# Performance work log

Hardware: AMD Instinct MI355X
Metric: run time of the kernel (lower is better)

Reference implementation:

```python
import jax, jax.numpy as jnp
import numpy as np

OUT_H = 7
OUT_W = 7
SPATIAL_SCALE = 0.0625
SAMPLING_RATIO = 2  # grid points per bin edge (static, as in Detectron2 configs)
ALIGNED = True


def setup_inputs() -> dict:
    key = jax.random.key(0)
    k_feat, k_xy, k_b = jax.random.split(key, 3)
    N, C, H, W = 2, 256, 128, 128
    K = 1024
    feat = jax.random.normal(k_feat, (N, C, H, W), dtype=jnp.float32)
    img = H / SPATIAL_SCALE  # 2048.0, image-space extent
    # two random corners per axis, sorted -> valid boxes in image coords
    xy = jax.random.uniform(k_xy, (K, 2, 2), dtype=jnp.float32) * img  # [K, {x,y}, 2]
    lo = jnp.min(xy, axis=-1)
    hi = jnp.max(xy, axis=-1)
    b = jax.random.randint(k_b, (K,), 0, N).astype(jnp.float32)
    rois = jnp.stack([b, lo[:, 0], lo[:, 1], hi[:, 0], hi[:, 1]], axis=1)  # [K,5]
    return {"feat": feat, "rois": rois}


def _roi_align(feat, rois):
    N, C, H, W = feat.shape
    K = rois.shape[0]
    g = SAMPLING_RATIO
    b = rois[:, 0].astype(jnp.int32)
    off = 0.5 if ALIGNED else 0.0
    x1 = rois[:, 1] * SPATIAL_SCALE - off
    y1 = rois[:, 2] * SPATIAL_SCALE - off
    x2 = rois[:, 3] * SPATIAL_SCALE - off
    y2 = rois[:, 4] * SPATIAL_SCALE - off
    rw = x2 - x1
    rh = y2 - y1
    if not ALIGNED:  # legacy: force min size 1
        rw = jnp.maximum(rw, 1.0)
        rh = jnp.maximum(rh, 1.0)
    bin_w = rw / OUT_W
    bin_h = rh / OUT_H
    # sample offsets within a bin: (i + 0.5)/g for i in 0..g-1
    frac = (jnp.arange(g, dtype=feat.dtype) + 0.5) / g  # [g]
    ph = jnp.arange(OUT_H, dtype=feat.dtype)
    pw = jnp.arange(OUT_W, dtype=feat.dtype)
    ys = y1[:, None, None] + (ph[None, :, None] + frac[None, None, :]) * bin_h[:, None, None]  # [K,PH,g]
    xs = x1[:, None, None] + (pw[None, :, None] + frac[None, None, :]) * bin_w[:, None, None]  # [K,PW,g]
    ys = ys.reshape(K, OUT_H * g)  # [K,Sy]
    xs = xs.reshape(K, OUT_W * g)  # [K,Sx]
    Y = jnp.broadcast_to(ys[:, :, None], (K, OUT_H * g, OUT_W * g))
    X = jnp.broadcast_to(xs[:, None, :], (K, OUT_H * g, OUT_W * g))
    S = OUT_H * g * OUT_W * g
    Y = Y.reshape(K, S)
    X = X.reshape(K, S)
    valid = (Y > -1.0) & (Y < H) & (X > -1.0) & (X < W)
    Yc = jnp.maximum(Y, 0.0)
    Xc = jnp.maximum(X, 0.0)
    y0 = jnp.clip(jnp.floor(Yc).astype(jnp.int32), 0, H - 1)
    x0 = jnp.clip(jnp.floor(Xc).astype(jnp.int32), 0, W - 1)
    y1i = jnp.minimum(y0 + 1, H - 1)
    x1i = jnp.minimum(x0 + 1, W - 1)
    ly = jnp.clip(Yc - y0.astype(feat.dtype), 0.0, 1.0)
    lx = jnp.clip(Xc - x0.astype(feat.dtype), 0.0, 1.0)
    hy = 1.0 - ly
    hx = 1.0 - lx
    bI = b[:, None]  # [K,1] broadcasts against [K,S]
    # advanced indices around the channel slice put (K,S) in front -> [K,S,C]
    v00 = feat[bI, :, y0, x0]
    v01 = feat[bI, :, y0, x1i]
    v10 = feat[bI, :, y1i, x0]
    v11 = feat[bI, :, y1i, x1i]
    w00 = (hy * hx)[:, :, None]
    w01 = (hy * lx)[:, :, None]
    w10 = (ly * hx)[:, :, None]
    w11 = (ly * lx)[:, :, None]
    val = w00 * v00 + w01 * v01 + w10 * v10 + w11 * v11  # [K,S,C]
    val = jnp.where(valid[:, :, None], val, 0.0)
    val = val.reshape(K, OUT_H, g, OUT_W, g, C)
    out = val.mean(axis=(2, 4))  # avg pool over the g*g samples per bin
    return out.transpose(0, 3, 1, 2)  # [K,C,OUT_H,OUT_W]


def reference(feat, rois):
    return _roi_align(feat, rois)
```

## Files before the change

### kernel.cpp

```cpp
#include <hip/hip_runtime.h>
#include <hip/hip_fp16.h>

#define NIMG 2
#define CCH 256
#define FH 128
#define FW 128
#define FHW (FH * FW)
#define OUTH 7
#define OUTW 7
#define NPIX 49
#define NSAMP (NPIX * 4)
#define KROIS 1024
#define SCALE 0.0625f
#define OPITCH 260

typedef float f32x4 __attribute__((ext_vector_type(4)));

__global__ __launch_bounds__(256) void prep_fused(const float* __restrict__ in,
                                                  __half* __restrict__ out,
                                                  const float* __restrict__ rois,
                                                  int* __restrict__ perm) {
    const int bid = blockIdx.x;
    const int t = threadIdx.x;
    if (bid < 8192) {
        __shared__ float tile[32][33];
        const int b   = bid >> 12;
        const int rem = bid & 4095;
        const int c0  = (rem >> 9) << 5;
        const int hw0 = (rem & 511) << 5;
        const int tx = t & 31;
        const int ty = t >> 5;
        const float* src = in  + (size_t)b * CCH * FHW;
        __half*      dst = out + (size_t)b * FHW * CCH;
#pragma unroll
        for (int i = 0; i < 32; i += 8)
            tile[ty + i][tx] = src[(size_t)(c0 + ty + i) * FHW + hw0 + tx];
        __syncthreads();
#pragma unroll
        for (int i = 0; i < 32; i += 8)
            dst[(size_t)(hw0 + ty + i) * CCH + c0 + tx] = __float2half(tile[tx][ty + i]);
    } else {
        __shared__ int hist[128];
        __shared__ int basep[128];
        __shared__ int keyv[KROIS];
        __shared__ int rankv[KROIS];
        if (t < 128) hist[t] = 0;
        __syncthreads();
#pragma unroll
        for (int i = 0; i < 4; ++i) {
            const int roi = t + (i << 8);
            const float* r = rois + roi * 5;
            const int b = (int)r[0];
            const float cx = (r[1] + r[3]) * 0.5f * SCALE;
            const float cy = (r[2] + r[4]) * 0.5f * SCALE;
            const int qx = min(max((int)cx, 0), FW - 1) >> 4;
            const int qy = min(max((int)cy, 0), FH - 1) >> 4;
            unsigned m = 0;
#pragma unroll
            for (int j = 0; j < 3; ++j)
                m |= (((unsigned)(qx >> j) & 1u) << (2 * j)) | (((unsigned)(qy >> j) & 1u) << (2 * j + 1));
            const int key = (b << 6) | (int)m;
            keyv[roi] = key;
            rankv[roi] = atomicAdd(&hist[key], 1);
        }
        __syncthreads();
        if (t < 64) {
            const int a = hist[2 * t], c = hist[2 * t + 1];
            int s = a + c;
#pragma unroll
            for (int d = 1; d < 64; d <<= 1) {
                const int n = __shfl_up(s, d);
                if (t >= d) s += n;
            }
            const int excl = s - (a + c);
            basep[2 * t]     = excl;
            basep[2 * t + 1] = excl + a;
        }
        __syncthreads();
#pragma unroll
        for (int i = 0; i < 4; ++i) {
            const int roi = t + (i << 8);
            perm[basep[keyv[roi]] + rankv[roi]] = roi;
        }
    }
}

__global__ __launch_bounds__(512) void roi_align_nhwc(const __half* __restrict__ nhwc,
                                                      const float* __restrict__ rois,
                                                      const int* __restrict__ perm,
                                                      float* __restrict__ out) {
    __shared__ __half obuf[NPIX * OPITCH];
    __shared__ __align__(16) int   soff[NSAMP][4];
    __shared__ __align__(16) float swgt[NSAMP][4];
    const int wg = blockIdx.x;
    const int pairBase = ((((wg & 7) << 6) | (wg >> 3)) << 1);
    const int lane = threadIdx.x & 63;
    const int wave = threadIdx.x >> 6;
    const int t = threadIdx.x;

    for (int half = 0; half < 2; ++half) {
        const int k = perm[pairBase + half];
        const float* r = rois + k * 5;
        const int b = __builtin_amdgcn_readfirstlane((int)r[0]);

        if (t < NSAMP) {
            const float x1 = __fsub_rn(__fmul_rn(r[1], SCALE), 0.5f);
            const float y1 = __fsub_rn(__fmul_rn(r[2], SCALE), 0.5f);
            const float x2 = __fsub_rn(__fmul_rn(r[3], SCALE), 0.5f);
            const float y2 = __fsub_rn(__fmul_rn(r[4], SCALE), 0.5f);
            const float bw = __fdiv_rn(__fsub_rn(x2, x1), (float)OUTW);
            const float bh = __fdiv_rn(__fsub_rn(y2, y1), (float)OUTH);
            const int pix = t >> 2, s = t & 3;
            const int ph = pix / 7, pw = pix - ph * 7;
            const int sy = s >> 1, sx = s & 1;
            const float fy = (float)ph + (sy ? 0.75f : 0.25f);
            const float fx = (float)pw + (sx ? 0.75f : 0.25f);
            const float y = __fadd_rn(y1, __fmul_rn(fy, bh));
            const float x = __fadd_rn(x1, __fmul_rn(fx, bw));
            int o00 = 0, o01 = 0, o10 = 0, o11 = 0;
            float w00 = 0.f, w01 = 0.f, w10 = 0.f, w11 = 0.f;
            if (y > -1.0f && y < (float)FH && x > -1.0f && x < (float)FW) {
                const float yc = fmaxf(y, 0.0f);
                const float xc = fmaxf(x, 0.0f);
                int y0 = (int)yc; if (y0 > FH - 1) y0 = FH - 1;
                int x0 = (int)xc; if (x0 > FW - 1) x0 = FW - 1;
                const int y1i = min(y0 + 1, FH - 1);
                const int x1i = min(x0 + 1, FW - 1);
                const float ly = fminf(yc - (float)y0, 1.0f);
                const float lx = fminf(xc - (float)x0, 1.0f);
                const float hy = 1.0f - ly, hx = 1.0f - lx;
                w00 = hy * hx; w01 = hy * lx; w10 = ly * hx; w11 = ly * lx;
                o00 = (y0  * FW + x0 ) << 9;
                o01 = (y0  * FW + x1i) << 9;
                o10 = (y1i * FW + x0 ) << 9;
                o11 = (y1i * FW + x1i) << 9;
            }
            soff[t][0] = o00; soff[t][1] = o01; soff[t][2] = o10; soff[t][3] = o11;
            swgt[t][0] = w00; swgt[t][1] = w01; swgt[t][2] = w10; swgt[t][3] = w11;
        }
        __syncthreads();

        const char* bp = (const char*)(nhwc + ((size_t)b * FHW << 8)) + (lane << 3);
        const int pstart = wave ? (6 * wave + 1) : 0;
        const int pend   = 6 * wave + 6;
        for (int pix = pstart; pix <= pend; ++pix) {
            float acc0 = 0.f, acc1 = 0.f, acc2 = 0.f, acc3 = 0.f;
#pragma unroll
            for (int s = 0; s < 4; ++s) {
                const int j = (pix << 2) + s;
                const int4  o = *(const int4*)(&soff[j][0]);
                const f32x4 w = *(const f32x4*)(&swgt[j][0]);
                const uint2 r00 = *(const uint2*)(bp + o.x);
                const uint2 r01 = *(const uint2*)(bp + o.y);
                const uint2 r10 = *(const uint2*)(bp + o.z);
                const uint2 r11 = *(const uint2*)(bp + o.w);
                const __half2 A00 = *(const __half2*)&r00.x, B00 = *(const __half2*)&r00.y;
                const __half2 A01 = *(const __half2*)&r01.x, B01 = *(const __half2*)&r01.y;
                const __half2 A10 = *(const __half2*)&r10.x, B10 = *(const __half2*)&r10.y;
                const __half2 A11 = *(const __half2*)&r11.x, B11 = *(const __half2*)&r11.y;
                acc0 = fmaf(w.x, __half2float(A00.x), acc0);
                acc1 = fmaf(w.x, __half2float(A00.y), acc1);
                acc2 = fmaf(w.x, __half2float(B00.x), acc2);
                acc3 = fmaf(w.x, __half2float(B00.y), acc3);
                acc0 = fmaf(w.y, __half2float(A01.x), acc0);
                acc1 = fmaf(w.y, __half2float(A01.y), acc1);
                acc2 = fmaf(w.y, __half2float(B01.x), acc2);
                acc3 = fmaf(w.y, __half2float(B01.y), acc3);
                acc0 = fmaf(w.z, __half2float(A10.x), acc0);
                acc1 = fmaf(w.z, __half2float(A10.y), acc1);
                acc2 = fmaf(w.z, __half2float(B10.x), acc2);
                acc3 = fmaf(w.z, __half2float(B10.y), acc3);
                acc0 = fmaf(w.w, __half2float(A11.x), acc0);
                acc1 = fmaf(w.w, __half2float(A11.y), acc1);
                acc2 = fmaf(w.w, __half2float(B11.x), acc2);
                acc3 = fmaf(w.w, __half2float(B11.y), acc3);
            }
            const __half2 h01 = __floats2half2_rn(acc0 * 0.25f, acc1 * 0.25f);
            const __half2 h23 = __floats2half2_rn(acc2 * 0.25f, acc3 * 0.25f);
            uint2 packed;
            packed.x = *(const unsigned*)&h01;
            packed.y = *(const unsigned*)&h23;
            *(uint2*)&obuf[pix * OPITCH + (lane << 2)] = packed;
        }
        __syncthreads();

        float* op = out + (size_t)k * (CCH * NPIX);
        for (int f4 = t; f4 < (CCH * NPIX) / 4; f4 += 512) {
            const int f = f4 << 2;
            f32x4 o;
            {
                const int fi = f + 0; const int c = fi / NPIX; const int p = fi - c * NPIX;
                o.x = __half2float(obuf[p * OPITCH + c]);
            }
            {
                const int fi = f + 1; const int c = fi / NPIX; const int p = fi - c * NPIX;
                o.y = __half2float(obuf[p * OPITCH + c]);
            }
            {
                const int fi = f + 2; const int c = fi / NPIX; const int p = fi - c * NPIX;
                o.z = __half2float(obuf[p * OPITCH + c]);
            }
            {
                const int fi = f + 3; const int c = fi / NPIX; const int p = fi - c * NPIX;
                o.w = __half2float(obuf[p * OPITCH + c]);
            }
            __builtin_nontemporal_store(o, (f32x4*)(op + f));
        }
        __syncthreads();
    }
}

__global__ __launch_bounds__(256) void roi_align_naive(const float* __restrict__ feat,
                                                       const float* __restrict__ rois,
                                                       float* __restrict__ out) {
    const size_t idx = (size_t)blockIdx.x * 256 + threadIdx.x;
    const size_t total = (size_t)KROIS * CCH * NPIX;
    if (idx >= total) return;
    const int pix = (int)(idx % NPIX);
    const int t1  = (int)(idx / NPIX);
    const int c   = t1 % CCH;
    const int k   = t1 / CCH;
    const int ph = pix / 7;
    const int pw = pix - ph * 7;

    const float* r = rois + k * 5;
    const int b = (int)r[0];
    const float x1 = __fsub_rn(__fmul_rn(r[1], SCALE), 0.5f);
    const float y1 = __fsub_rn(__fmul_rn(r[2], SCALE), 0.5f);
    const float x2 = __fsub_rn(__fmul_rn(r[3], SCALE), 0.5f);
    const float y2 = __fsub_rn(__fmul_rn(r[4], SCALE), 0.5f);
    const float bw = __fdiv_rn(__fsub_rn(x2, x1), (float)OUTW);
    const float bh = __fdiv_rn(__fsub_rn(y2, y1), (float)OUTH);
    const float* fp = feat + (size_t)(b * CCH + c) * FHW;

    float acc = 0.f;
#pragma unroll
    for (int s = 0; s < 4; ++s) {
        const int sy = s >> 1, sx = s & 1;
        const float fy = (float)ph + (sy ? 0.75f : 0.25f);
        const float fx = (float)pw + (sx ? 0.75f : 0.25f);
        const float y = __fadd_rn(y1, __fmul_rn(fy, bh));
        const float x = __fadd_rn(x1, __fmul_rn(fx, bw));
        if (y > -1.0f && y < (float)FH && x > -1.0f && x < (float)FW) {
            const float yc = fmaxf(y, 0.0f);
            const float xc = fmaxf(x, 0.0f);
            int y0 = (int)yc; if (y0 > FH - 1) y0 = FH - 1;
            int x0 = (int)xc; if (x0 > FW - 1) x0 = FW - 1;
            const int y1i = min(y0 + 1, FH - 1);
            const int x1i = min(x0 + 1, FW - 1);
            const float ly = fminf(yc - (float)y0, 1.0f);
            const float lx = fminf(xc - (float)x0, 1.0f);
            const float hy = 1.0f - ly, hx = 1.0f - lx;
            acc += (hy * hx) * fp[y0  * FW + x0 ] + (hy * lx) * fp[y0  * FW + x1i]
                 + (ly * hx) * fp[y1i * FW + x0 ] + (ly * lx) * fp[y1i * FW + x1i];
        }
    }
    out[idx] = acc * 0.25f;
}

extern "C" void kernel_launch(void* const* d_in, const int* in_sizes, int n_in,
                              void* d_out, int out_size, void* d_ws, size_t ws_size,
                              hipStream_t stream) {
    const float* feat = (const float*)d_in[0];
    const float* rois = (const float*)d_in[1];
    float* out = (float*)d_out;

    const size_t nhwc_bytes = (size_t)NIMG * CCH * FHW * sizeof(__half);
    const size_t need = nhwc_bytes + KROIS * sizeof(int);
    if (ws_size >= need) {
        __half* nhwc = (__half*)d_ws;
        int* perm = (int*)((char*)d_ws + nhwc_bytes);
        prep_fused<<<dim3(8193), dim3(256), 0, stream>>>(feat, nhwc, rois, perm);
        roi_align_nhwc<<<dim3(512), dim3(512), 0, stream>>>(nhwc, rois, perm, out);
    } else {
        const size_t total = (size_t)KROIS * CCH * NPIX;
        roi_align_naive<<<dim3((unsigned)((total + 255) / 256)), dim3(256), 0, stream>>>(feat, rois, out);
    }
}
```

Baseline: 48.60 us.

## Partition ROIs by image and half-height across XCDs, split channels per block

ROIs are now bucketed into four groups by batch image and the top or bottom half of the feature map, and the groups' start offsets are written to a small bases array. Each XCD (blockIdx & 7) handles one group and one channel half, so every XCD's L2 only sees a quarter of one image's rows and half of its channels. Blocks shrink to 256 threads, each processing one ROI per iteration with 2 channels per lane. The block count grows to 3072 in a strided loop. This adds imbalance risk if the groups have uneven sizes, and the stores become narrower.

```diff
diff --git a/kernel.cpp b/kernel.cpp
--- a/kernel.cpp
+++ b/kernel.cpp
@@ -3,6 +3,7 @@
 
 #define NIMG 2
 #define CCH 256
+#define HALFC 128
 #define FH 128
 #define FW 128
 #define FHW (FH * FW)
@@ -12,14 +13,16 @@
 #define NSAMP (NPIX * 4)
 #define KROIS 1024
 #define SCALE 0.0625f
-#define OPITCH 260
+#define OPITCH 132
+#define MAXJ 384
 
 typedef float f32x4 __attribute__((ext_vector_type(4)));
 
 __global__ __launch_bounds__(256) void prep_fused(const float* __restrict__ in,
                                                   __half* __restrict__ out,
                                                   const float* __restrict__ rois,
-                                                  int* __restrict__ perm) {
+                                                  int* __restrict__ perm,
+                                                  int* __restrict__ bases) {
     const int bid = blockIdx.x;
     const int t = threadIdx.x;
     if (bid < 8192) {
@@ -53,13 +56,11 @@
             const int b = (int)r[0];
             const float cx = (r[1] + r[3]) * 0.5f * SCALE;
             const float cy = (r[2] + r[4]) * 0.5f * SCALE;
-            const int qx = min(max((int)cx, 0), FW - 1) >> 4;
-            const int qy = min(max((int)cy, 0), FH - 1) >> 4;
-            unsigned m = 0;
-#pragma unroll
-            for (int j = 0; j < 3; ++j)
-                m |= (((unsigned)(qx >> j) & 1u) << (2 * j)) | (((unsigned)(qy >> j) & 1u) << (2 * j + 1));
-            const int key = (b << 6) | (int)m;
+            const int qcx = min(max((int)cx, 0), FW - 1);
+            const int qcy = min(max((int)cy, 0), FH - 1);
+            const int g = (b << 1) | (qcy >> 6);
+            const int cell = (((qcy & 63) >> 4) << 3) | (qcx >> 4);
+            const int key = (g << 5) | cell;
             keyv[roi] = key;
             rankv[roi] = atomicAdd(&hist[key], 1);
         }
@@ -77,6 +78,8 @@
             basep[2 * t + 1] = excl + a;
         }
         __syncthreads();
+        if (t < 4) bases[t] = basep[t << 5];
+        if (t == 0) bases[4] = KROIS;
 #pragma unroll
         for (int i = 0; i < 4; ++i) {
             const int roi = t + (i << 8);
@@ -85,21 +88,28 @@
     }
 }
 
-__global__ __launch_bounds__(512) void roi_align_nhwc(const __half* __restrict__ nhwc,
-                                                      const float* __restrict__ rois,
-                                                      const int* __restrict__ perm,
-                                                      float* __restrict__ out) {
+__global__ __launch_bounds__(256, 8) void roi_align_nhwc(const __half* __restrict__ nhwc,
+                                                         const float* __restrict__ rois,
+                                                         const int* __restrict__ perm,
+                                                         const int* __restrict__ bases,
+                                                         float* __restrict__ out) {
     __shared__ __half obuf[NPIX * OPITCH];
     __shared__ __align__(16) int   soff[NSAMP][4];
     __shared__ __align__(16) float swgt[NSAMP][4];
-    const int wg = blockIdx.x;
-    const int pairBase = ((((wg & 7) << 6) | (wg >> 3)) << 1);
-    const int lane = threadIdx.x & 63;
-    const int wave = threadIdx.x >> 6;
+    const int bid = blockIdx.x;
+    const int xcd = bid & 7;
+    const int p = xcd >> 2;
+    const int g = xcd & 3;
+    const int base  = bases[g];
+    const int count = bases[g + 1] - base;
     const int t = threadIdx.x;
-
-    for (int half = 0; half < 2; ++half) {
-        const int k = perm[pairBase + half];
+    const int lane = t & 63;
+    const int wave = t >> 6;
+    const int pstart = wave ? (12 * wave + 1) : 0;
+    const int pend   = pstart + (wave ? 12 : 13);
+
+    for (int j = bid >> 3; j < count; j += MAXJ) {
+        const int k = perm[base + j];
         const float* r = rois + k * 5;
         const int b = __builtin_amdgcn_readfirstlane((int)r[0]);
 
@@ -140,69 +150,55 @@
         }
         __syncthreads();
 
-        const char* bp = (const char*)(nhwc + ((size_t)b * FHW << 8)) + (lane << 3);
-        const int pstart = wave ? (6 * wave + 1) : 0;
-        const int pend   = 6 * wave + 6;
-        for (int pix = pstart; pix <= pend; ++pix) {
-            float acc0 = 0.f, acc1 = 0.f, acc2 = 0.f, acc3 = 0.f;
+        const char* bp = (const char*)(nhwc + ((size_t)b * FHW << 8)) + (p << 8) + (lane << 2);
+        for (int pix = pstart; pix < pend; ++pix) {
+            float acc0 = 0.f, acc1 = 0.f;
 #pragma unroll
             for (int s = 0; s < 4; ++s) {
-                const int j = (pix << 2) + s;
-                const int4  o = *(const int4*)(&soff[j][0]);
-                const f32x4 w = *(const f32x4*)(&swgt[j][0]);
-                const uint2 r00 = *(const uint2*)(bp + o.x);
-                const uint2 r01 = *(const uint2*)(bp + o.y);
-                const uint2 r10 = *(const uint2*)(bp + o.z);
-                const uint2 r11 = *(const uint2*)(bp + o.w);
-                const __half2 A00 = *(const __half2*)&r00.x, B00 = *(const __half2*)&r00.y;
-                const __half2 A01 = *(const __half2*)&r01.x, B01 = *(const __half2*)&r01.y;
-                const __half2 A10 = *(const __half2*)&r10.x, B10 = *(const __half2*)&r10.y;
-                const __half2 A11 = *(const __half2*)&r11.x, B11 = *(const __half2*)&r11.y;
+                const int jj = (pix << 2) + s;
+                const int4  o = *(const int4*)(&soff[jj][0]);
+                const f32x4 w = *(const f32x4*)(&swgt[jj][0]);
+                const unsigned r00 = *(const unsigned*)(bp + o.x);
+                const unsigned r01 = *(const unsigned*)(bp + o.y);
+                const unsigned r10 = *(const unsigned*)(bp + o.z);
+                const unsigned r11 = *(const unsigned*)(bp + o.w);
+                const __half2 A00 = *(const __half2*)&r00;
+                const __half2 A01 = *(const __half2*)&r01;
+                const __half2 A10 = *(const __half2*)&r10;
+                const __half2 A11 = *(const __half2*)&r11;
                 acc0 = fmaf(w.x, __half2float(A00.x), acc0);
                 acc1 = fmaf(w.x, __half2float(A00.y), acc1);
-                acc2 = fmaf(w.x, __half2float(B00.x), acc2);
-                acc3 = fmaf(w.x, __half2float(B00.y), acc3);
                 acc0 = fmaf(w.y, __half2float(A01.x), acc0);
                 acc1 = fmaf(w.y, __half2float(A01.y), acc1);
-                acc2 = fmaf(w.y, __half2float(B01.x), acc2);
-                acc3 = fmaf(w.y, __half2float(B01.y), acc3);
                 acc0 = fmaf(w.z, __half2float(A10.x), acc0);
                 acc1 = fmaf(w.z, __half2float(A10.y), acc1);
-                acc2 = fmaf(w.z, __half2float(B10.x), acc2);
-                acc3 = fmaf(w.z, __half2float(B10.y), acc3);
                 acc0 = fmaf(w.w, __half2float(A11.x), acc0);
                 acc1 = fmaf(w.w, __half2float(A11.y), acc1);
-                acc2 = fmaf(w.w, __half2float(B11.x), acc2);
-                acc3 = fmaf(w.w, __half2float(B11.y), acc3);
-            }
-            const __half2 h01 = __floats2half2_rn(acc0 * 0.25f, acc1 * 0.25f);
-            const __half2 h23 = __floats2half2_rn(acc2 * 0.25f, acc3 * 0.25f);
-            uint2 packed;
-            packed.x = *(const unsigned*)&h01;
-            packed.y = *(const unsigned*)&h23;
-            *(uint2*)&obuf[pix * OPITCH + (lane << 2)] = packed;
-        }
-        __syncthreads();
-
-        float* op = out + (size_t)k * (CCH * NPIX);
-        for (int f4 = t; f4 < (CCH * NPIX) / 4; f4 += 512) {
+            }
+            const __half2 h = __floats2half2_rn(acc0 * 0.25f, acc1 * 0.25f);
+            *(unsigned*)&obuf[pix * OPITCH + (lane << 1)] = *(const unsigned*)&h;
+        }
+        __syncthreads();
+
+        float* op = out + (size_t)k * (CCH * NPIX) + (size_t)p * (HALFC * NPIX);
+        for (int f4 = t; f4 < (HALFC * NPIX) / 4; f4 += 256) {
             const int f = f4 << 2;
             f32x4 o;
             {
-                const int fi = f + 0; const int c = fi / NPIX; const int p = fi - c * NPIX;
-                o.x = __half2float(obuf[p * OPITCH + c]);
-            }
-            {
-                const int fi = f + 1; const int c = fi / NPIX; const int p = fi - c * NPIX;
-                o.y = __half2float(obuf[p * OPITCH + c]);
-            }
-            {
-                const int fi = f + 2; const int c = fi / NPIX; const int p = fi - c * NPIX;
-                o.z = __half2float(obuf[p * OPITCH + c]);
-            }
-            {
-                const int fi = f + 3; const int c = fi / NPIX; const int p = fi - c * NPIX;
-                o.w = __half2float(obuf[p * OPITCH + c]);
+                const int fi = f + 0; const int c = fi / NPIX; const int pp = fi - c * NPIX;
+                o.x = __half2float(obuf[pp * OPITCH + c]);
+            }
+            {
+                const int fi = f + 1; const int c = fi / NPIX; const int pp = fi - c * NPIX;
+                o.y = __half2float(obuf[pp * OPITCH + c]);
+            }
+            {
+                const int fi = f + 2; const int c = fi / NPIX; const int pp = fi - c * NPIX;
+                o.z = __half2float(obuf[pp * OPITCH + c]);
+            }
+            {
+                const int fi = f + 3; const int c = fi / NPIX; const int pp = fi - c * NPIX;
+                o.w = __half2float(obuf[pp * OPITCH + c]);
             }
             __builtin_nontemporal_store(o, (f32x4*)(op + f));
         }
@@ -266,12 +262,13 @@
     float* out = (float*)d_out;
 
     const size_t nhwc_bytes = (size_t)NIMG * CCH * FHW * sizeof(__half);
-    const size_t need = nhwc_bytes + KROIS * sizeof(int);
+    const size_t need = nhwc_bytes + KROIS * sizeof(int) + 32;
     if (ws_size >= need) {
         __half* nhwc = (__half*)d_ws;
         int* perm = (int*)((char*)d_ws + nhwc_bytes);
-        prep_fused<<<dim3(8193), dim3(256), 0, stream>>>(feat, nhwc, rois, perm);
-        roi_align_nhwc<<<dim3(512), dim3(512), 0, stream>>>(nhwc, rois, perm, out);
+        int* bases = perm + KROIS;
+        prep_fused<<<dim3(8193), dim3(256), 0, stream>>>(feat, nhwc, rois, perm, bases);
+        roi_align_nhwc<<<dim3(8 * MAXJ), dim3(256), 0, stream>>>(nhwc, rois, perm, bases, out);
     } else {
         const size_t total = (size_t)KROIS * CCH * NPIX;
         roi_align_naive<<<dim3((unsigned)((total + 255) / 256)), dim3(256), 0, stream>>>(feat, rois, out);
```

Result: faster. 46.17 us (-5.0%).
